# Kernel tuning notes

Measured on AMD Instinct MI355X. Metric: run time of the kernel, lower is better.

The kernel has to match this reference:

```python
import jax, jax.numpy as jnp
import numpy as np

B, C, H, W = 8, 512, 96, 96
CQ = 64  # inter_ch


def setup_inputs() -> dict:
    key = jax.random.key(0)
    ks = jax.random.split(key, 8)
    scale = 1.0 / np.sqrt(C)
    return {
        "x": jax.random.normal(ks[0], (B, C, H, W), dtype=jnp.float32),
        "Wq": jax.random.normal(ks[1], (CQ, C), dtype=jnp.float32) * scale,
        "bq": jax.random.normal(ks[2], (CQ,), dtype=jnp.float32) * 0.01,
        "Wk": jax.random.normal(ks[3], (CQ, C), dtype=jnp.float32) * scale,
        "bk": jax.random.normal(ks[4], (CQ,), dtype=jnp.float32) * 0.01,
        "Wv": jax.random.normal(ks[5], (C, C), dtype=jnp.float32) * scale,
        "bv": jax.random.normal(ks[6], (C,), dtype=jnp.float32) * 0.01,
        "gamma": jax.random.normal(ks[7], (1,), dtype=jnp.float32) * 0.1,
    }


def reference(x, Wq, bq, Wk, bk, Wv, bv, gamma):
    # 1x1 convs expressed as channel matmuls; outputs in BHWC layout
    Q = jnp.einsum('bchw,oc->bhwo', x, Wq) + bq   # [B,H,W,CQ]
    K = jnp.einsum('bchw,oc->bhwo', x, Wk) + bk   # [B,H,W,CQ]
    V = jnp.einsum('bchw,oc->bhwo', x, Wv) + bv   # [B,H,W,C]

    # Per pixel (i,j): keys = concat(row i keys [W], column j keys [H]).
    # NOTE: this replication includes pixel (i,j) twice (once in row, once in col),
    # matching the torch loop exactly (no -INF masking as in original CCNet).
    e_row = jnp.einsum('bhwc,bhvc->bhwv', Q, K)   # [B,H,W,W] attend along row h
    e_col = jnp.einsum('bhwc,bgwc->bhwg', Q, K)   # [B,H,W,H] attend along col w
    attn = jax.nn.softmax(jnp.concatenate([e_row, e_col], axis=-1), axis=-1)
    a_row, a_col = attn[..., :W], attn[..., W:]   # [B,H,W,W], [B,H,W,H]

    out = (jnp.einsum('bhwv,bhvc->bhwc', a_row, V)
           + jnp.einsum('bhwg,bgwc->bhwc', a_col, V))  # [B,H,W,C]
    out = jnp.transpose(out, (0, 3, 1, 2))        # [B,C,H,W]
    return x + gamma[0] * out
```

## Files before the change

### kernel.cpp

```cpp
#include <hip/hip_runtime.h>
#include <stdint.h>

#define B_  8
#define C_  512
#define H_  96
#define W_  96
#define CQ_ 64
#define P_  (H_*W_)
#define NP  (B_*P_)
#define L_  (W_+H_)

typedef __attribute__((ext_vector_type(8))) short short8;
typedef __attribute__((ext_vector_type(4))) float f32x4;
typedef __attribute__((ext_vector_type(4))) unsigned short us4;

__device__ __forceinline__ ushort f2bf(float f) {
    uint32_t u = __builtin_bit_cast(uint32_t, f);
    u += 0x7fff + ((u >> 16) & 1);
    return (ushort)(u >> 16);
}
__device__ __forceinline__ float bf2f(ushort h) {
    uint32_t u = ((uint32_t)h) << 16;
    return __builtin_bit_cast(float, u);
}

#define GLL16(g, l) __builtin_amdgcn_global_load_lds( \
    (const __attribute__((address_space(1))) uint32_t*)(g), \
    (__attribute__((address_space(3))) uint32_t*)(l), 16, 0, 0)

#define FSW(r) (((r) >> 1) & 3)

__device__ __forceinline__ int TSW(int r, int c) {
    return r * 128 + ((((c >> 2) ^ ((r >> 2) & 7))) << 2) + (c & 3);
}

__global__ __launch_bounds__(256) void k_xt(const float* __restrict__ x, ushort* __restrict__ xt) {
    __shared__ float tile[64 * 67];
    int p0 = blockIdx.x * 64, c0 = blockIdx.y * 64, bat = blockIdx.z;
    int tid = threadIdx.x;
    const float* xb = x + ((size_t)bat * C_ + c0) * P_ + p0;
    #pragma unroll
    for (int k = 0; k < 4; ++k) {
        int u = tid + k * 256, row = u >> 4, p4 = (u & 15) * 4;
        float4 v = *(const float4*)&xb[(size_t)row * P_ + p4];
        tile[row * 67 + p4]     = v.x;
        tile[row * 67 + p4 + 1] = v.y;
        tile[row * 67 + p4 + 2] = v.z;
        tile[row * 67 + p4 + 3] = v.w;
    }
    __syncthreads();
    ushort* o = xt + ((size_t)bat * P_ + p0) * C_ + c0;
    #pragma unroll
    for (int k = 0; k < 4; ++k) {
        int u = tid + k * 256, p = u >> 4, c4 = (u & 15) * 4;
        us4 v;
        v.x = f2bf(tile[(c4 + 0) * 67 + p]);
        v.y = f2bf(tile[(c4 + 1) * 67 + p]);
        v.z = f2bf(tile[(c4 + 2) * 67 + p]);
        v.w = f2bf(tile[(c4 + 3) * 67 + p]);
        *(us4*)&o[(size_t)p * C_ + c4] = v;
    }
}

__global__ __launch_bounds__(256) void k_wconv(const float* __restrict__ Wq, const float* __restrict__ Wk,
                                               const float* __restrict__ Wv, const float* __restrict__ bq,
                                               const float* __restrict__ bk, const float* __restrict__ bv,
                                               ushort* __restrict__ Wall, float* __restrict__ ball) {
    int idx = blockIdx.x * 256 + threadIdx.x;
    if (idx < 640) {
        float b;
        if (idx < 64)       b = bq[idx];
        else if (idx < 128) b = bk[idx - 64];
        else                b = bv[idx - 128];
        ball[idx] = b;
    }
    if (idx >= 640 * C_) return;
    int o = idx / C_, c = idx % C_;
    float v;
    if (o < 64)       v = Wq[o * C_ + c];
    else if (o < 128) v = Wk[(o - 64) * C_ + c];
    else              v = Wv[(o - 128) * C_ + c];
    Wall[idx] = f2bf(v);
}

__global__ __launch_bounds__(256, 4) void k_proj(const ushort* __restrict__ xt, const ushort* __restrict__ Wall,
                                                 const float* __restrict__ ball,
                                                 ushort* __restrict__ Qb, ushort* __restrict__ Kb,
                                                 ushort* __restrict__ Vcm) {
    __shared__ __align__(16) ushort SB[2][2 * 128 * 32];
    ushort* Tl = &SB[0][0];
    int tid = threadIdx.x, lane = tid & 63, wv = tid >> 6;
    int wr = wv >> 1, wc = wv & 1;
    int wg = ((int)blockIdx.x & 7) * 360 + ((int)blockIdx.x >> 3);
    int m0 = (wg % 5) * 128;
    int n0 = (wg / 5) * 128;
    f32x4 acc[4][4] = {};
    {
        ushort* Al = &SB[0][0]; ushort* Bl = &SB[0][128 * 32];
        #pragma unroll
        for (int i = 0; i < 2; ++i) {
            int u = tid + i * 256, row = u >> 2, seg = u & 3;
            int sg = (seg ^ FSW(row)) << 3;
            GLL16(&Wall[(size_t)(m0 + row) * C_ + sg], &Al[(size_t)u * 8]);
            GLL16(&xt[(size_t)(n0 + row) * C_ + sg],   &Bl[(size_t)u * 8]);
        }
    }
    __syncthreads();
    for (int t = 0; t < 16; ++t) {
        int cur = t & 1;
        if (t < 15) {
            int kb = (t + 1) * 32;
            ushort* Al = &SB[cur ^ 1][0]; ushort* Bl = &SB[cur ^ 1][128 * 32];
            #pragma unroll
            for (int i = 0; i < 2; ++i) {
                int u = tid + i * 256, row = u >> 2, seg = u & 3;
                int sg = (seg ^ FSW(row)) << 3;
                GLL16(&Wall[(size_t)(m0 + row) * C_ + kb + sg], &Al[(size_t)u * 8]);
                GLL16(&xt[(size_t)(n0 + row) * C_ + kb + sg],   &Bl[(size_t)u * 8]);
            }
        }
        const ushort* Al = &SB[cur][0];
        const ushort* Bl = &SB[cur][128 * 32];
        int rr = lane & 15, gq = lane >> 4, ck = gq ^ FSW(rr);
        short8 fb[4];
        #pragma unroll
        for (int nt = 0; nt < 4; ++nt) fb[nt] = *(const short8*)&Bl[(wc * 64 + nt * 16 + rr) * 32 + ck * 8];
        #pragma unroll
        for (int mt = 0; mt < 4; ++mt) {
            short8 fa = *(const short8*)&Al[(wr * 64 + mt * 16 + rr) * 32 + ck * 8];
            #pragma unroll
            for (int nt = 0; nt < 4; ++nt)
                acc[mt][nt] = __builtin_amdgcn_mfma_f32_16x16x32_bf16(fa, fb[nt], acc[mt][nt], 0, 0, 0);
        }
        __syncthreads();
    }
    int rr = lane & 15, gq = lane >> 4;
    int bat = n0 / P_, pb0 = n0 - bat * P_;
    if (m0 == 0) {
        #pragma unroll
        for (int pass = 0; pass < 2; ++pass) {
            __syncthreads();
            if (wr == pass) {
                #pragma unroll
                for (int mt = 0; mt < 4; ++mt)
                    #pragma unroll
                    for (int nt = 0; nt < 4; ++nt) {
                        int col = wc * 64 + nt * 16 + rr;
                        #pragma unroll
                        for (int q = 0; q < 4; ++q) {
                            int ol = mt * 16 + gq * 4 + q;
                            Tl[col * 68 + ol] = f2bf(acc[mt][nt][q] + ball[pass * 64 + ol]);
                        }
                    }
            }
            __syncthreads();
            ushort* dst = pass ? Kb : Qb;
            int p = tid >> 1, off = (tid & 1) * 32;
            #pragma unroll
            for (int j = 0; j < 8; ++j)
                *(us4*)&dst[(size_t)(n0 + p) * CQ_ + off + j * 4] = *(const us4*)&Tl[p * 68 + off + j * 4];
        }
    } else {
        #pragma unroll
        for (int mt = 0; mt < 4; ++mt)
            #pragma unroll
            for (int nt = 0; nt < 4; ++nt) {
                int col = wc * 64 + nt * 16 + rr;
                #pragma unroll
                for (int q = 0; q < 4; ++q) {
                    int o = m0 + wr * 64 + mt * 16 + gq * 4 + q;
                    int c = o - 128;
                    Vcm[((size_t)bat * C_ + c) * P_ + pb0 + col] = f2bf(acc[mt][nt][q] + ball[o]);
                }
            }
    }
}

__global__ __launch_bounds__(256) void k_vt(const ushort* __restrict__ Vcm, ushort* __restrict__ Vt) {
    __shared__ ushort t[96 * 128];
    int c = blockIdx.x, bat = blockIdx.y;
    const ushort* src = Vcm + ((size_t)(bat * C_ + c)) * P_;
    int tid = threadIdx.x;
    #pragma unroll
    for (int k = 0; k < 9; ++k) {
        int u = tid + k * 256, h = u / 24, w4 = (u % 24) * 4;
        us4 v = *(const us4*)&src[h * 96 + w4];
        t[TSW(h, w4)]     = v.x;
        t[TSW(h, w4) + 1] = v.y;
        t[TSW(h, w4) + 2] = v.z;
        t[TSW(h, w4) + 3] = v.w;
    }
    __syncthreads();
    #pragma unroll
    for (int k = 0; k < 9; ++k) {
        int u = tid + k * 256, w = u / 24, h4 = (u % 24) * 4;
        us4 o;
        o.x = t[TSW(h4 + 0, w)];
        o.y = t[TSW(h4 + 1, w)];
        o.z = t[TSW(h4 + 2, w)];
        o.w = t[TSW(h4 + 3, w)];
        *(us4*)&Vt[((size_t)(bat * W_ + w) * C_ + c) * H_ + h4] = o;
    }
}

#define LSTR 40
__global__ __launch_bounds__(256) void k_erow(const ushort* __restrict__ Qb, const ushort* __restrict__ Kb,
                                              ushort* __restrict__ attn) {
    __shared__ __align__(16) ushort Al[96 * LSTR];
    __shared__ __align__(16) ushort Bl[96 * LSTR];
    int h = blockIdx.x, bat = blockIdx.y;
    int tid = threadIdx.x, lane = tid & 63, wvid = tid >> 6;
    int wr = wvid >> 1, wc = wvid & 1;
    size_t base = ((size_t)bat * H_ + h) * W_;
    f32x4 acc[3][3] = {};
    for (int kb = 0; kb < CQ_; kb += 32) {
        for (int s = tid; s < 96 * 4; s += 256) {
            int row = s >> 2, seg = s & 3;
            *(short8*)&Al[row * LSTR + seg * 8] = *(const short8*)&Qb[(base + row) * CQ_ + kb + seg * 8];
            *(short8*)&Bl[row * LSTR + seg * 8] = *(const short8*)&Kb[(base + row) * CQ_ + kb + seg * 8];
        }
        __syncthreads();
        int rr = lane & 15, gq = lane >> 4;
        #pragma unroll
        for (int mt = 0; mt < 3; ++mt) {
            short8 fa = *(const short8*)&Al[(wr * 48 + mt * 16 + rr) * LSTR + gq * 8];
            #pragma unroll
            for (int nt = 0; nt < 3; ++nt) {
                short8 fb = *(const short8*)&Bl[(wc * 48 + nt * 16 + rr) * LSTR + gq * 8];
                acc[mt][nt] = __builtin_amdgcn_mfma_f32_16x16x32_bf16(fa, fb, acc[mt][nt], 0, 0, 0);
            }
        }
        __syncthreads();
    }
    int rr = lane & 15, gq = lane >> 4;
    #pragma unroll
    for (int mt = 0; mt < 3; ++mt)
        #pragma unroll
        for (int nt = 0; nt < 3; ++nt)
            #pragma unroll
            for (int q = 0; q < 4; ++q) {
                int w = wr * 48 + mt * 16 + gq * 4 + q;
                int v = wc * 48 + nt * 16 + rr;
                attn[(base + w) * L_ + v] = f2bf(acc[mt][nt][q]);
            }
}

__global__ __launch_bounds__(256) void k_ecolsm(const ushort* __restrict__ Qb, const ushort* __restrict__ Kb,
                                                ushort* __restrict__ attn) {
    __shared__ __align__(16) ushort Al[96 * LSTR];
    __shared__ __align__(16) ushort Bl[96 * LSTR];
    __shared__ ushort ecl[96 * 100];
    int w = blockIdx.x, bat = blockIdx.y;
    int tid = threadIdx.x, lane = tid & 63, wvid = tid >> 6;
    int wr = wvid >> 1, wc = wvid & 1;
    f32x4 acc[3][3] = {};
    for (int kb = 0; kb < CQ_; kb += 32) {
        for (int s = tid; s < 96 * 4; s += 256) {
            int row = s >> 2, seg = s & 3;
            size_t px = ((size_t)bat * H_ + row) * W_ + w;
            *(short8*)&Al[row * LSTR + seg * 8] = *(const short8*)&Qb[px * CQ_ + kb + seg * 8];
            *(short8*)&Bl[row * LSTR + seg * 8] = *(const short8*)&Kb[px * CQ_ + kb + seg * 8];
        }
        __syncthreads();
        int rr = lane & 15, gq = lane >> 4;
        #pragma unroll
        for (int mt = 0; mt < 3; ++mt) {
            short8 fa = *(const short8*)&Al[(wr * 48 + mt * 16 + rr) * LSTR + gq * 8];
            #pragma unroll
            for (int nt = 0; nt < 3; ++nt) {
                short8 fb = *(const short8*)&Bl[(wc * 48 + nt * 16 + rr) * LSTR + gq * 8];
                acc[mt][nt] = __builtin_amdgcn_mfma_f32_16x16x32_bf16(fa, fb, acc[mt][nt], 0, 0, 0);
            }
        }
        __syncthreads();
    }
    {
        int rr = lane & 15, gq = lane >> 4;
        #pragma unroll
        for (int mt = 0; mt < 3; ++mt)
            #pragma unroll
            for (int nt = 0; nt < 3; ++nt)
                #pragma unroll
                for (int q = 0; q < 4; ++q) {
                    int hh = wr * 48 + mt * 16 + gq * 4 + q;
                    int gg = wc * 48 + nt * 16 + rr;
                    ecl[hh * 100 + gg] = f2bf(acc[mt][nt][q]);
                }
    }
    __syncthreads();
    for (int h = wvid; h < H_; h += 4) {
        size_t pix = ((size_t)bat * H_ + h) * W_ + w;
        ushort* ap = attn + pix * L_;
        float a  = bf2f(ap[lane]);
        float b  = (lane < 32) ? bf2f(ap[64 + lane]) : -1e30f;
        float c0 = bf2f(ecl[h * 100 + lane]);
        float c1 = (lane < 32) ? bf2f(ecl[h * 100 + 64 + lane]) : -1e30f;
        float m = fmaxf(fmaxf(a, b), fmaxf(c0, c1));
        #pragma unroll
        for (int off = 32; off; off >>= 1) m = fmaxf(m, __shfl_xor(m, off));
        float ea = __expf(a - m), eb = (lane < 32) ? __expf(b - m) : 0.0f;
        float ec0 = __expf(c0 - m), ec1 = (lane < 32) ? __expf(c1 - m) : 0.0f;
        float s = ea + eb + ec0 + ec1;
        #pragma unroll
        for (int off = 32; off; off >>= 1) s += __shfl_xor(s, off);
        float inv = 1.0f / s;
        ap[lane] = f2bf(ea * inv);
        ap[96 + lane] = f2bf(ec0 * inv);
        if (lane < 32) {
            ap[64 + lane] = f2bf(eb * inv);
            ap[160 + lane] = f2bf(ec1 * inv);
        }
    }
}

__global__ __launch_bounds__(512) void k_pvcol(const ushort* __restrict__ Vt, const ushort* __restrict__ attn,
                                               ushort* __restrict__ out1t) {
    __shared__ __align__(16) ushort Al[512 * 32];
    __shared__ __align__(16) ushort Bl[96 * 32];
    int w = blockIdx.x, bat = blockIdx.y;
    int tid = threadIdx.x, lane = tid & 63, wvid = tid >> 6;
    int wrm = wvid >> 1, wcn = wvid & 1;
    size_t vbase = ((size_t)bat * W_ + w) * C_ * H_;
    size_t abase = ((size_t)bat * P_ + w) * L_ + W_;
    f32x4 acc[8][3] = {};
    for (int kb = 0; kb < 96; kb += 32) {
        #pragma unroll
        for (int i = 0; i < 4; ++i) {
            int u = tid + i * 512, row = u >> 2, seg = u & 3;
            int sg = (seg ^ FSW(row)) << 3;
            GLL16(&Vt[vbase + (size_t)row * H_ + kb + sg], &Al[(size_t)u * 8]);
        }
        if (tid < 384) {
            int row = tid >> 2, seg = tid & 3;
            int sg = (seg ^ FSW(row)) << 3;
            GLL16(&attn[abase + (size_t)row * (W_ * L_) + kb + sg], &Bl[(size_t)tid * 8]);
        }
        __syncthreads();
        int rr = lane & 15, gq = lane >> 4, ck = gq ^ FSW(rr);
        short8 fb[3];
        #pragma unroll
        for (int nt = 0; nt < 3; ++nt) fb[nt] = *(const short8*)&Bl[(wcn * 48 + nt * 16 + rr) * 32 + ck * 8];
        #pragma unroll
        for (int mt = 0; mt < 8; ++mt) {
            short8 fa = *(const short8*)&Al[(wrm * 128 + mt * 16 + rr) * 32 + ck * 8];
            #pragma unroll
            for (int nt = 0; nt < 3; ++nt)
                acc[mt][nt] = __builtin_amdgcn_mfma_f32_16x16x32_bf16(fa, fb[nt], acc[mt][nt], 0, 0, 0);
        }
        __syncthreads();
    }
    int rr = lane & 15, gq = lane >> 4;
    #pragma unroll
    for (int mt = 0; mt < 8; ++mt)
        #pragma unroll
        for (int nt = 0; nt < 3; ++nt) {
            int hh = wcn * 48 + nt * 16 + rr;
            #pragma unroll
            for (int q = 0; q < 4; ++q) {
                int c = wrm * 128 + mt * 16 + gq * 4 + q;
                out1t[((size_t)(bat * C_ + c) * W_ + w) * H_ + hh] = f2bf(acc[mt][nt][q]);
            }
        }
}

__global__ __launch_bounds__(512) void k_pvrow(const ushort* __restrict__ Vcm, const ushort* __restrict__ attn,
                                               ushort* __restrict__ out0) {
    __shared__ __align__(16) ushort Al[512 * 32];
    __shared__ __align__(16) ushort Bl[96 * 32];
    int h = blockIdx.x, bat = blockIdx.y;
    int tid = threadIdx.x, lane = tid & 63, wvid = tid >> 6;
    int wrm = wvid >> 1, wcn = wvid & 1;
    size_t vbase = (size_t)bat * C_ * P_ + (size_t)h * W_;
    size_t abase = ((size_t)bat * H_ + h) * W_ * L_;
    f32x4 acc[8][3] = {};
    for (int kb = 0; kb < 96; kb += 32) {
        #pragma unroll
        for (int i = 0; i < 4; ++i) {
            int u = tid + i * 512, row = u >> 2, seg = u & 3;
            int sg = (seg ^ FSW(row)) << 3;
            GLL16(&Vcm[vbase + (size_t)row * P_ + kb + sg], &Al[(size_t)u * 8]);
        }
        if (tid < 384) {
            int row = tid >> 2, seg = tid & 3;
            int sg = (seg ^ FSW(row)) << 3;
            GLL16(&attn[abase + (size_t)row * L_ + kb + sg], &Bl[(size_t)tid * 8]);
        }
        __syncthreads();
        int rr = lane & 15, gq = lane >> 4, ck = gq ^ FSW(rr);
        short8 fb[3];
        #pragma unroll
        for (int nt = 0; nt < 3; ++nt) fb[nt] = *(const short8*)&Bl[(wcn * 48 + nt * 16 + rr) * 32 + ck * 8];
        #pragma unroll
        for (int mt = 0; mt < 8; ++mt) {
            short8 fa = *(const short8*)&Al[(wrm * 128 + mt * 16 + rr) * 32 + ck * 8];
            #pragma unroll
            for (int nt = 0; nt < 3; ++nt)
                acc[mt][nt] = __builtin_amdgcn_mfma_f32_16x16x32_bf16(fa, fb[nt], acc[mt][nt], 0, 0, 0);
        }
        __syncthreads();
    }
    int rr = lane & 15, gq = lane >> 4;
    #pragma unroll
    for (int mt = 0; mt < 8; ++mt)
        #pragma unroll
        for (int nt = 0; nt < 3; ++nt) {
            int w = wcn * 48 + nt * 16 + rr;
            #pragma unroll
            for (int q = 0; q < 4; ++q) {
                int c = wrm * 128 + mt * 16 + gq * 4 + q;
                out0[((size_t)bat * C_ + c) * P_ + (size_t)h * W_ + w] = f2bf(acc[mt][nt][q]);
            }
        }
}

__global__ __launch_bounds__(256) void k_final(const float* __restrict__ x, const ushort* __restrict__ out0,
                                               const ushort* __restrict__ out1t, const float* __restrict__ gamma,
                                               float* __restrict__ out) {
    __shared__ ushort t[96 * 128];
    int c = blockIdx.x, bat = blockIdx.y;
    const ushort* src = out1t + ((size_t)bat * C_ + c) * P_;
    int tid = threadIdx.x;
    #pragma unroll
    for (int k = 0; k < 9; ++k) {
        int u = tid + k * 256, w = u / 24, h4 = (u % 24) * 4;
        us4 v = *(const us4*)&src[w * 96 + h4];
        t[TSW(h4 + 0, w)] = v.x;
        t[TSW(h4 + 1, w)] = v.y;
        t[TSW(h4 + 2, w)] = v.z;
        t[TSW(h4 + 3, w)] = v.w;
    }
    __syncthreads();
    float gm = gamma[0];
    size_t base = ((size_t)bat * C_ + c) * P_;
    #pragma unroll
    for (int k = 0; k < 9; ++k) {
        int u = tid + k * 256, h = u / 24, w4 = (u % 24) * 4;
        size_t idx = base + h * W_ + w4;
        float4 xv = *(const float4*)&x[idx];
        us4 o0 = *(const us4*)&out0[idx];
        us4 o1 = *(const us4*)&t[TSW(h, w4)];
        float4 r;
        r.x = xv.x + gm * (bf2f(o0.x) + bf2f(o1.x));
        r.y = xv.y + gm * (bf2f(o0.y) + bf2f(o1.y));
        r.z = xv.z + gm * (bf2f(o0.z) + bf2f(o1.z));
        r.w = xv.w + gm * (bf2f(o0.w) + bf2f(o1.w));
        *(float4*)&out[idx] = r;
    }
}

extern "C" void kernel_launch(void* const* d_in, const int* in_sizes, int n_in,
                              void* d_out, int out_size, void* d_ws, size_t ws_size,
                              hipStream_t stream) {
    const float* x     = (const float*)d_in[0];
    const float* Wq    = (const float*)d_in[1];
    const float* bq    = (const float*)d_in[2];
    const float* Wk    = (const float*)d_in[3];
    const float* bk    = (const float*)d_in[4];
    const float* Wv    = (const float*)d_in[5];
    const float* bv    = (const float*)d_in[6];
    const float* gamma = (const float*)d_in[7];
    float* out = (float*)d_out;
    char* ws = (char*)d_ws;

    const size_t SZ  = (size_t)NP * C_ * 2;
    const size_t QKS = (size_t)NP * CQ_ * 2;
    ushort* xt     = (ushort*)(ws);
    ushort* out1t  = (ushort*)(ws);
    ushort* Vcm    = (ushort*)(ws + SZ);
    ushort* Vt     = (ushort*)(ws + 2 * SZ);
    ushort* out0   = Vt;
    ushort* Qb     = (ushort*)(ws + 3 * SZ);
    ushort* Kb     = (ushort*)(ws + 3 * SZ + QKS);
    ushort* attn   = (ushort*)(ws + 3 * SZ + 2 * QKS);
    size_t off_wall = 3 * SZ + 2 * QKS + (size_t)NP * L_ * 2;
    ushort* Wall   = (ushort*)(ws + off_wall);
    float*  ball   = (float*) (ws + off_wall + 640 * C_ * 2);

    k_wconv  <<<dim3(1280),       dim3(256),   0, stream>>>(Wq, Wk, Wv, bq, bk, bv, Wall, ball);
    k_xt     <<<dim3(144, 8, 8),  dim3(256),   0, stream>>>(x, xt);
    k_proj   <<<dim3(2880),       dim3(256),   0, stream>>>(xt, Wall, ball, Qb, Kb, Vcm);
    k_vt     <<<dim3(512, 8),     dim3(256),   0, stream>>>(Vcm, Vt);
    k_erow   <<<dim3(96, 8),      dim3(256),   0, stream>>>(Qb, Kb, attn);
    k_ecolsm <<<dim3(96, 8),      dim3(256),   0, stream>>>(Qb, Kb, attn);
    k_pvcol  <<<dim3(96, 8),      dim3(512),   0, stream>>>(Vt, attn, out1t);
    k_pvrow  <<<dim3(96, 8),      dim3(512),   0, stream>>>(Vcm, attn, out0);
    k_final  <<<dim3(512, 8),     dim3(256),   0, stream>>>(x, out0, out1t, gamma, out);
}
```

Baseline: 349.5 us.

## Double-buffer LDS tiles in PV column and row kernels

Converts the k-loop of the two attention-times-V kernels into a two-stage LDS ping-pong, issuing global-to-LDS loads for the next 32-wide K chunk before computing on the current chunk. This aims to overlap load latency with MFMA work, since each kernel has only three K iterations. LDS use roughly doubles (about 76 KB per block), which may lower occupancy. With so few iterations, little latency can be hidden.

```diff
diff --git a/kernel.cpp b/kernel.cpp
--- a/kernel.cpp
+++ b/kernel.cpp
@@ -313,29 +313,51 @@
     }
 }
 
+#define PVA (512 * 32)
+#define PVB (96 * 32)
 __global__ __launch_bounds__(512) void k_pvcol(const ushort* __restrict__ Vt, const ushort* __restrict__ attn,
                                                ushort* __restrict__ out1t) {
-    __shared__ __align__(16) ushort Al[512 * 32];
-    __shared__ __align__(16) ushort Bl[96 * 32];
+    __shared__ __align__(16) ushort SB[2][PVA + PVB];
     int w = blockIdx.x, bat = blockIdx.y;
     int tid = threadIdx.x, lane = tid & 63, wvid = tid >> 6;
     int wrm = wvid >> 1, wcn = wvid & 1;
     size_t vbase = ((size_t)bat * W_ + w) * C_ * H_;
     size_t abase = ((size_t)bat * P_ + w) * L_ + W_;
     f32x4 acc[8][3] = {};
-    for (int kb = 0; kb < 96; kb += 32) {
+    {
+        ushort* Al = &SB[0][0]; ushort* Bl = &SB[0][PVA];
         #pragma unroll
         for (int i = 0; i < 4; ++i) {
             int u = tid + i * 512, row = u >> 2, seg = u & 3;
             int sg = (seg ^ FSW(row)) << 3;
-            GLL16(&Vt[vbase + (size_t)row * H_ + kb + sg], &Al[(size_t)u * 8]);
+            GLL16(&Vt[vbase + (size_t)row * H_ + sg], &Al[(size_t)u * 8]);
         }
         if (tid < 384) {
             int row = tid >> 2, seg = tid & 3;
             int sg = (seg ^ FSW(row)) << 3;
-            GLL16(&attn[abase + (size_t)row * (W_ * L_) + kb + sg], &Bl[(size_t)tid * 8]);
-        }
-        __syncthreads();
+            GLL16(&attn[abase + (size_t)row * (W_ * L_) + sg], &Bl[(size_t)tid * 8]);
+        }
+    }
+    __syncthreads();
+    for (int t = 0; t < 3; ++t) {
+        int cur = t & 1;
+        if (t < 2) {
+            int kb = (t + 1) * 32;
+            ushort* Al = &SB[cur ^ 1][0]; ushort* Bl = &SB[cur ^ 1][PVA];
+            #pragma unroll
+            for (int i = 0; i < 4; ++i) {
+                int u = tid + i * 512, row = u >> 2, seg = u & 3;
+                int sg = (seg ^ FSW(row)) << 3;
+                GLL16(&Vt[vbase + (size_t)row * H_ + kb + sg], &Al[(size_t)u * 8]);
+            }
+            if (tid < 384) {
+                int row = tid >> 2, seg = tid & 3;
+                int sg = (seg ^ FSW(row)) << 3;
+                GLL16(&attn[abase + (size_t)row * (W_ * L_) + kb + sg], &Bl[(size_t)tid * 8]);
+            }
+        }
+        const ushort* Al = &SB[cur][0];
+        const ushort* Bl = &SB[cur][PVA];
         int rr = lane & 15, gq = lane >> 4, ck = gq ^ FSW(rr);
         short8 fb[3];
         #pragma unroll
@@ -365,27 +387,47 @@
 
 __global__ __launch_bounds__(512) void k_pvrow(const ushort* __restrict__ Vcm, const ushort* __restrict__ attn,
                                                ushort* __restrict__ out0) {
-    __shared__ __align__(16) ushort Al[512 * 32];
-    __shared__ __align__(16) ushort Bl[96 * 32];
+    __shared__ __align__(16) ushort SB[2][PVA + PVB];
     int h = blockIdx.x, bat = blockIdx.y;
     int tid = threadIdx.x, lane = tid & 63, wvid = tid >> 6;
     int wrm = wvid >> 1, wcn = wvid & 1;
     size_t vbase = (size_t)bat * C_ * P_ + (size_t)h * W_;
     size_t abase = ((size_t)bat * H_ + h) * W_ * L_;
     f32x4 acc[8][3] = {};
-    for (int kb = 0; kb < 96; kb += 32) {
+    {
+        ushort* Al = &SB[0][0]; ushort* Bl = &SB[0][PVA];
         #pragma unroll
         for (int i = 0; i < 4; ++i) {
             int u = tid + i * 512, row = u >> 2, seg = u & 3;
             int sg = (seg ^ FSW(row)) << 3;
-            GLL16(&Vcm[vbase + (size_t)row * P_ + kb + sg], &Al[(size_t)u * 8]);
+            GLL16(&Vcm[vbase + (size_t)row * P_ + sg], &Al[(size_t)u * 8]);
         }
         if (tid < 384) {
             int row = tid >> 2, seg = tid & 3;
             int sg = (seg ^ FSW(row)) << 3;
-            GLL16(&attn[abase + (size_t)row * L_ + kb + sg], &Bl[(size_t)tid * 8]);
-        }
-        __syncthreads();
+            GLL16(&attn[abase + (size_t)row * L_ + sg], &Bl[(size_t)tid * 8]);
+        }
+    }
+    __syncthreads();
+    for (int t = 0; t < 3; ++t) {
+        int cur = t & 1;
+        if (t < 2) {
+            int kb = (t + 1) * 32;
+            ushort* Al = &SB[cur ^ 1][0]; ushort* Bl = &SB[cur ^ 1][PVA];
+            #pragma unroll
+            for (int i = 0; i < 4; ++i) {
+                int u = tid + i * 512, row = u >> 2, seg = u & 3;
+                int sg = (seg ^ FSW(row)) << 3;
+                GLL16(&Vcm[vbase + (size_t)row * P_ + kb + sg], &Al[(size_t)u * 8]);
+            }
+            if (tid < 384) {
+                int row = tid >> 2, seg = tid & 3;
+                int sg = (seg ^ FSW(row)) << 3;
+                GLL16(&attn[abase + (size_t)row * L_ + kb + sg], &Bl[(size_t)tid * 8]);
+            }
+        }
+        const ushort* Al = &SB[cur][0];
+        const ushort* Bl = &SB[cur][PVA];
         int rr = lane & 15, gq = lane >> 4, ck = gq ^ FSW(rr);
         short8 fb[3];
         #pragma unroll
```

New measurement: 349.1 us. Within noise of the previous version (-0.1%).
